# Performance work log

Hardware: AMD Instinct MI355X
Metric: run time of the kernel (lower is better)

The kernel has to match this reference:

```python
import jax, jax.numpy as jnp
import numpy as np

B, T, F = 256, 784, 1
H, D, C = 256, 1024, 10  # cell_size, dense_size, num_classes


def setup_inputs() -> dict:
    key = jax.random.key(0)
    ks = jax.random.split(key, 5)
    s = 0.05
    return {
        "X": jax.random.normal(ks[0], (B, T, F), jnp.float32),
        "W_lstm": jax.random.normal(ks[1], (F + H, 4 * H), jnp.float32) * s,
        "b_lstm": jnp.zeros((4 * H,), jnp.float32),
        "W_dense": jax.random.normal(ks[2], (H, D), jnp.float32) * s,
        "b_dense": jnp.zeros((D,), jnp.float32),
        "W_pred": jax.random.normal(ks[3], (D, C), jnp.float32) * s,
        "b_pred": jnp.zeros((C,), jnp.float32),
        "seq_length": T,
    }


def reference(X, W_lstm, b_lstm, W_dense, b_dense, W_pred, b_pred, seq_length):
    # TF LSTMCell: kernel [F+H, 4H], gate order (i, j, f, o), forget_bias=1.0
    b, t, f = X.shape
    h4 = W_lstm.shape[1]
    h = h4 // 4
    Wx, Wh = W_lstm[:f], W_lstm[f:]
    # Precompute input projections for all timesteps: [T, B, 4H]
    xproj = jnp.einsum('tbf,fg->tbg', jnp.transpose(X, (1, 0, 2)), Wx) + b_lstm

    def step(carry, xp):
        c, hst = carry
        gates = xp + hst @ Wh  # [B, 4H]
        i, j, fg, o = jnp.split(gates, 4, axis=-1)
        new_c = jax.nn.sigmoid(fg + 1.0) * c + jax.nn.sigmoid(i) * jnp.tanh(j)
        new_h = jax.nn.sigmoid(o) * jnp.tanh(new_c)
        return (new_c, new_h), None

    init = (jnp.zeros((b, h), X.dtype), jnp.zeros((b, h), X.dtype))
    (_, h_last), _ = jax.lax.scan(step, init, xproj)

    # Dropout in inference mode = identity
    dense = jax.nn.relu(h_last @ W_dense + b_dense)
    logits = dense @ W_pred + b_pred
    return logits
```

## Files before the change

### kernel.cpp

```cpp
#include <hip/hip_runtime.h>
#include <stdint.h>

#define TSEQ  784
#define BATCH 256
#define HID   256
#define DNS   1024
#define NCLS  10
#define NGRP  16
#define NSLC  8

typedef __attribute__((ext_vector_type(8))) short bf16x8_t;
typedef __attribute__((ext_vector_type(4))) float f32x4_t;

__device__ __forceinline__ float sigmoidf_(float x) { return 1.0f / (1.0f + __expf(-x)); }
__device__ __forceinline__ float tanhf_(float x) {
    float ax = fabsf(x);
    float e  = __expf(2.0f * ax);
    float r  = 1.0f - 2.0f / (e + 1.0f);
    return copysignf(r, x);
}
__device__ __forceinline__ uint32_t bf16rne(float f) {
    uint32_t u = __float_as_uint(f);
    return (u + 0x7FFFu + ((u >> 16) & 1u)) >> 16;
}
__device__ __forceinline__ float bf16tof(uint32_t h) { return __uint_as_float(h << 16); }

__global__ __launch_bounds__(256, 1)
void lstm_mfma(const float* __restrict__ X,
               const float* __restrict__ W_lstm,
               const float* __restrict__ b_lstm,
               uint32_t* __restrict__ hx,
               uint32_t* __restrict__ tags)
{
    __shared__ uint32_t WtU[32768];
    __shared__ uint32_t hA[4096];
    __shared__ float    gateL[4 * 32 * 17];

    const int tid  = threadIdx.x;
    const int lane = tid & 63;
    const int wid  = tid >> 6;
    const int cidx = lane & 15;
    const int kh   = lane >> 4;

    const int bid = blockIdx.x;
    const int s   = bid >> 4;
    const int g   = bid & 15;

    for (int idx = tid; idx < 8 * 16 * 128; idx += 256) {
        const int n  = idx >> 11;
        const int c  = (idx >> 7) & 15;
        const int dw = idx & 127;
        const int k0 = dw * 2;
        const int col = (n >> 1) * 256 + s * 32 + (n & 1) * 16 + c;
        const float w0 = W_lstm[(1 + k0) * 1024 + col];
        const float w1 = W_lstm[(2 + k0) * 1024 + col];
        const uint32_t h0 = bf16rne(w0), h1 = bf16rne(w1);
        const uint32_t l0 = bf16rne(w0 - bf16tof(h0));
        const uint32_t l1 = bf16rne(w1 - bf16tof(h1));
        const int kc = dw >> 2, rem = dw & 3;
        const int dwp = ((kc ^ (c & 7)) << 2) | rem;
        const int o = (n * 16 + c) * 128 + dwp;
        WtU[o]         = h0 | (h1 << 16);
        WtU[16384 + o] = l0 | (l1 << 16);
    }

    const int er = tid >> 4;
    const int eu = tid & 15;
    float wx0[4], wx1[4], bb0[4], bb1[4];
    #pragma unroll
    for (int q = 0; q < 4; ++q) {
        const int c0 = q * 256 + s * 32 + eu;
        wx0[q] = W_lstm[c0];      wx1[q] = W_lstm[c0 + 16];
        bb0[q] = b_lstm[c0];      bb1[q] = b_lstm[c0 + 16];
    }
    const float* xrow = X + (g * 16 + er) * TSEQ;
    float cc0 = 0.0f, cc1 = 0.0f;

    const int key = (cidx + (cidx >> 2)) & 3;
    const int kq  = (kh ^ key) << 2;

    __syncthreads();

    bf16x8_t Bh0[8], Bl0[8], Bh1[8], Bl1[8];
    #pragma unroll
    for (int kt = 0; kt < 8; ++kt) {
        const int kc  = kt * 4 + kh;
        const int ob0 = ((wid * 2) * 16 + cidx) * 128 + ((kc ^ (cidx & 7)) << 2);
        const int ob1 = ((wid * 2 + 1) * 16 + cidx) * 128 + ((kc ^ (cidx & 7)) << 2);
        Bh0[kt] = *reinterpret_cast<const bf16x8_t*>(&WtU[ob0]);
        Bl0[kt] = *reinterpret_cast<const bf16x8_t*>(&WtU[16384 + ob0]);
        Bh1[kt] = *reinterpret_cast<const bf16x8_t*>(&WtU[ob1]);
        Bl1[kt] = *reinterpret_cast<const bf16x8_t*>(&WtU[16384 + ob1]);
    }

    for (int t = 0; t < TSEQ; ++t) {
        #pragma unroll
        for (int kt = 0; kt < 8; kt += 4) {
            asm volatile("" : "+v"(Bh0[kt]), "+v"(Bh0[kt+1]), "+v"(Bh0[kt+2]), "+v"(Bh0[kt+3]),
                              "+v"(Bl0[kt]), "+v"(Bl0[kt+1]), "+v"(Bl0[kt+2]), "+v"(Bl0[kt+3]));
            asm volatile("" : "+v"(Bh1[kt]), "+v"(Bh1[kt+1]), "+v"(Bh1[kt+2]), "+v"(Bh1[kt+3]),
                              "+v"(Bl1[kt]), "+v"(Bl1[kt+1]), "+v"(Bl1[kt+2]), "+v"(Bl1[kt+3]));
        }

        if (t > 0 && wid == 0) {
            const uint32_t tt = (uint32_t)t;
            int guard = 1 << 22;
            bool ok;
            do {
                uint32_t v = __hip_atomic_load(&tags[g * 8 + (lane & 7)],
                                               __ATOMIC_RELAXED, __HIP_MEMORY_SCOPE_AGENT);
                ok = __all(v >= tt);
            } while (!ok && --guard);
        }
        __syncthreads();

        {
            const int bufr = t & 1;
            const unsigned long long* src =
                (const unsigned long long*)hx + (size_t)(bufr * NGRP + g) * 2048;
            unsigned long long v[8];
            #pragma unroll
            for (int j = 0; j < 8; ++j) {
                v[j] = __hip_atomic_load(&src[j * 256 + tid],
                                         __ATOMIC_RELAXED, __HIP_MEMORY_SCOPE_AGENT);
            }
            #pragma unroll
            for (int j = 0; j < 8; ++j) {
                const int m   = j * 256 + tid;
                const int kt  = m >> 8;
                const int lvl = (m >> 7) & 1;
                const int ci  = (m & 127) >> 3;
                const int ko  = (m & 7) * 2;
                const int khj = ko >> 2, dp = ko & 3;
                const int kyj = (ci + (ci >> 2)) & 3;
                const int dst = kt * 512 + lvl * 256 + ci * 16 + ((khj ^ kyj) << 2) + dp;
                *(unsigned long long*)&hA[dst] = v[j];
            }
        }
        __syncthreads();

        f32x4_t acc0 = {0.f, 0.f, 0.f, 0.f}, acc1 = acc0;
        #pragma unroll
        for (int kt = 0; kt < 8; ++kt) {
            bf16x8_t av_h = *reinterpret_cast<const bf16x8_t*>(&hA[kt * 512 + cidx * 16 + kq]);
            bf16x8_t av_l = *reinterpret_cast<const bf16x8_t*>(&hA[kt * 512 + 256 + cidx * 16 + kq]);
            acc0 = __builtin_amdgcn_mfma_f32_16x16x32_bf16(av_h, Bh0[kt], acc0, 0, 0, 0);
            acc0 = __builtin_amdgcn_mfma_f32_16x16x32_bf16(av_h, Bl0[kt], acc0, 0, 0, 0);
            acc0 = __builtin_amdgcn_mfma_f32_16x16x32_bf16(av_l, Bh0[kt], acc0, 0, 0, 0);
            acc1 = __builtin_amdgcn_mfma_f32_16x16x32_bf16(av_h, Bh1[kt], acc1, 0, 0, 0);
            acc1 = __builtin_amdgcn_mfma_f32_16x16x32_bf16(av_h, Bl1[kt], acc1, 0, 0, 0);
            acc1 = __builtin_amdgcn_mfma_f32_16x16x32_bf16(av_l, Bh1[kt], acc1, 0, 0, 0);
        }

        #pragma unroll
        for (int reg = 0; reg < 4; ++reg) {
            gateL[(wid * 32 + cidx) * 17      + kh * 4 + reg] = acc0[reg];
            gateL[(wid * 32 + 16 + cidx) * 17 + kh * 4 + reg] = acc1[reg];
        }
        __syncthreads();

        const float xv = xrow[t];
        float g0[4], g1[4];
        #pragma unroll
        for (int q = 0; q < 4; ++q) {
            g0[q] = gateL[(q * 32 + eu) * 17 + er]      + xv * wx0[q] + bb0[q];
            g1[q] = gateL[(q * 32 + 16 + eu) * 17 + er] + xv * wx1[q] + bb1[q];
        }
        cc0 = fmaf(sigmoidf_(g0[2] + 1.0f), cc0, sigmoidf_(g0[0]) * tanhf_(g0[1]));
        const float h0 = sigmoidf_(g0[3]) * tanhf_(cc0);
        cc1 = fmaf(sigmoidf_(g1[2] + 1.0f), cc1, sigmoidf_(g1[0]) * tanhf_(g1[1]));
        const float h1 = sigmoidf_(g1[3]) * tanhf_(cc1);

        const float h0n = __shfl_xor(h0, 1, 64);
        const float h1n = __shfl_xor(h1, 1, 64);
        if ((eu & 1) == 0) {
            const int bufw  = (t + 1) & 1;
            const int basew = ((bufw * NGRP + g) * NSLC + s) * 512 + er * 16;
            const uint32_t hi0 = bf16rne(h0),  hi0n = bf16rne(h0n);
            const uint32_t hi1 = bf16rne(h1),  hi1n = bf16rne(h1n);
            const uint32_t lo0  = bf16rne(h0  - bf16tof(hi0));
            const uint32_t lo0n = bf16rne(h0n - bf16tof(hi0n));
            const uint32_t lo1  = bf16rne(h1  - bf16tof(hi1));
            const uint32_t lo1n = bf16rne(h1n - bf16tof(hi1n));
            const int D0 = eu >> 1, D1 = 8 + (eu >> 1);
            __hip_atomic_store(&hx[basew + D0], hi0 | (hi0n << 16),
                               __ATOMIC_RELAXED, __HIP_MEMORY_SCOPE_AGENT);
            __hip_atomic_store(&hx[basew + D1], hi1 | (hi1n << 16),
                               __ATOMIC_RELAXED, __HIP_MEMORY_SCOPE_AGENT);
            __hip_atomic_store(&hx[basew + 256 + D0], lo0 | (lo0n << 16),
                               __ATOMIC_RELAXED, __HIP_MEMORY_SCOPE_AGENT);
            __hip_atomic_store(&hx[basew + 256 + D1], lo1 | (lo1n << 16),
                               __ATOMIC_RELAXED, __HIP_MEMORY_SCOPE_AGENT);
        }
        __syncthreads();
        if (tid == 0) {
            __hip_atomic_store(&tags[g * 8 + s], (uint32_t)(t + 1),
                               __ATOMIC_RELAXED, __HIP_MEMORY_SCOPE_AGENT);
        }
    }
}

__global__ __launch_bounds__(256, 1)
void head_kernel(const uint32_t* __restrict__ hx,
                 const float* __restrict__ W_dense,
                 const float* __restrict__ b_dense,
                 const float* __restrict__ W_pred,
                 const float* __restrict__ b_pred,
                 float* __restrict__ out) {
    __shared__ float hs[HID];
    __shared__ float ds[DNS];
    __shared__ float red[4];

    const int b = blockIdx.x;
    const int g = b >> 4, er = b & 15;
    const int tid = threadIdx.x;

    {
        const int s  = tid >> 5;
        const int uu = tid & 31;
        const int base = (g * NSLC + s) * 512 + er * 16;
        const uint32_t dh = __hip_atomic_load(&hx[base + (uu >> 1)],
                                              __ATOMIC_RELAXED, __HIP_MEMORY_SCOPE_AGENT);
        const uint32_t dl = __hip_atomic_load(&hx[base + 256 + (uu >> 1)],
                                              __ATOMIC_RELAXED, __HIP_MEMORY_SCOPE_AGENT);
        const int sh = (uu & 1) * 16;
        hs[tid] = bf16tof((dh >> sh) & 0xFFFFu) + bf16tof((dl >> sh) & 0xFFFFu);
    }
    __syncthreads();

    for (int d = tid; d < DNS; d += 256) {
        float acc = b_dense[d];
        for (int k = 0; k < HID; k += 4) {
            float4 h4 = *reinterpret_cast<const float4*>(&hs[k]);
            acc = fmaf(h4.x, W_dense[(k + 0) * DNS + d], acc);
            acc = fmaf(h4.y, W_dense[(k + 1) * DNS + d], acc);
            acc = fmaf(h4.z, W_dense[(k + 2) * DNS + d], acc);
            acc = fmaf(h4.w, W_dense[(k + 3) * DNS + d], acc);
        }
        ds[d] = fmaxf(acc, 0.0f);
    }
    __syncthreads();

    const int wid = tid >> 6, lane = tid & 63;
    for (int c = 0; c < NCLS; ++c) {
        float p = 0.0f;
        for (int k = tid; k < DNS; k += 256) {
            p = fmaf(ds[k], W_pred[k * NCLS + c], p);
        }
        #pragma unroll
        for (int off = 32; off > 0; off >>= 1) {
            p += __shfl_down(p, off, 64);
        }
        if (lane == 0) red[wid] = p;
        __syncthreads();
        if (tid == 0) {
            out[b * NCLS + c] = red[0] + red[1] + red[2] + red[3] + b_pred[c];
        }
        __syncthreads();
    }
}

extern "C" void kernel_launch(void* const* d_in, const int* in_sizes, int n_in,
                              void* d_out, int out_size, void* d_ws, size_t ws_size,
                              hipStream_t stream) {
    const float* X       = (const float*)d_in[0];
    const float* W_lstm  = (const float*)d_in[1];
    const float* b_lstm  = (const float*)d_in[2];
    const float* W_dense = (const float*)d_in[3];
    const float* b_dense = (const float*)d_in[4];
    const float* W_pred  = (const float*)d_in[5];
    const float* b_pred  = (const float*)d_in[6];
    float* out = (float*)d_out;

    uint32_t* hx   = (uint32_t*)d_ws;
    uint32_t* tags = hx + 131072;

    hipMemsetAsync(hx, 0, NGRP * NSLC * 512 * sizeof(uint32_t), stream);
    hipMemsetAsync(tags, 0, NGRP * NSLC * sizeof(uint32_t), stream);

    lstm_mfma<<<NGRP * NSLC, 256, 0, stream>>>(X, W_lstm, b_lstm, hx, tags);
    head_kernel<<<BATCH, 256, 0, stream>>>(hx, W_dense, b_dense, W_pred, b_pred, out);
}
```

Baseline: 2.127 ms.

## Transpose gate accumulators in registers via lane shuffles instead of LDS round-trip

Reorders the recurrent weight columns so that each MFMA output tile holds all four gates for a small set of units. A 4x4 register transpose built from cross-lane shuffles then gives each lane its i/j/f/o values directly. This removes the shared-memory gate staging buffer and one block-wide barrier per timestep on the serial recurrence. In exchange it adds shuffle and select instructions and changes which lane owns which batch row and unit.

```diff
diff --git a/kernel.cpp b/kernel.cpp
--- a/kernel.cpp
+++ b/kernel.cpp
@@ -24,6 +24,30 @@
     return (u + 0x7FFFu + ((u >> 16) & 1u)) >> 16;
 }
 __device__ __forceinline__ float bf16tof(uint32_t h) { return __uint_as_float(h << 16); }
+
+__device__ __forceinline__ f32x4_t xpose44(f32x4_t M, int p) {
+    const bool pb1 = (p & 2) != 0;
+    float s0 = pb1 ? M[0] : M[2];
+    float s1 = pb1 ? M[1] : M[3];
+    float r0 = __shfl_xor(s0, 8, 64);
+    float r1 = __shfl_xor(s1, 8, 64);
+    f32x4_t N;
+    N[0] = pb1 ? r0 : M[0];
+    N[1] = pb1 ? r1 : M[1];
+    N[2] = pb1 ? M[2] : r0;
+    N[3] = pb1 ? M[3] : r1;
+    const bool pb0 = (p & 1) != 0;
+    s0 = pb0 ? N[0] : N[1];
+    s1 = pb0 ? N[2] : N[3];
+    r0 = __shfl_xor(s0, 4, 64);
+    r1 = __shfl_xor(s1, 4, 64);
+    f32x4_t T;
+    T[0] = pb0 ? r0 : N[0];
+    T[1] = pb0 ? N[1] : r0;
+    T[2] = pb0 ? r1 : N[2];
+    T[3] = pb0 ? N[3] : r1;
+    return T;
+}
 
 __global__ __launch_bounds__(256, 1)
 void lstm_mfma(const float* __restrict__ X,
@@ -34,7 +58,6 @@
 {
     __shared__ uint32_t WtU[32768];
     __shared__ uint32_t hA[4096];
-    __shared__ float    gateL[4 * 32 * 17];
 
     const int tid  = threadIdx.x;
     const int lane = tid & 63;
@@ -51,7 +74,7 @@
         const int c  = (idx >> 7) & 15;
         const int dw = idx & 127;
         const int k0 = dw * 2;
-        const int col = (n >> 1) * 256 + s * 32 + (n & 1) * 16 + c;
+        const int col = (c >> 2) * 256 + s * 32 + n * 4 + (c & 3);
         const float w0 = W_lstm[(1 + k0) * 1024 + col];
         const float w1 = W_lstm[(2 + k0) * 1024 + col];
         const uint32_t h0 = bf16rne(w0), h1 = bf16rne(w1);
@@ -64,17 +87,20 @@
         WtU[16384 + o] = l0 | (l1 << 16);
     }
 
-    const int er = tid >> 4;
-    const int eu = tid & 15;
-    float wx0[4], wx1[4], bb0[4], bb1[4];
+    const int p     = cidx >> 2;
+    const int row   = kh * 4 + p;
+    const int unitA = 8 * wid + (cidx & 3);
+    const int unitB = unitA + 4;
+    float wxA[4], wxB[4], bbA[4], bbB[4];
     #pragma unroll
     for (int q = 0; q < 4; ++q) {
-        const int c0 = q * 256 + s * 32 + eu;
-        wx0[q] = W_lstm[c0];      wx1[q] = W_lstm[c0 + 16];
-        bb0[q] = b_lstm[c0];      bb1[q] = b_lstm[c0 + 16];
-    }
-    const float* xrow = X + (g * 16 + er) * TSEQ;
-    float cc0 = 0.0f, cc1 = 0.0f;
+        wxA[q] = W_lstm[q * 256 + s * 32 + unitA];
+        wxB[q] = W_lstm[q * 256 + s * 32 + unitB];
+        bbA[q] = b_lstm[q * 256 + s * 32 + unitA];
+        bbB[q] = b_lstm[q * 256 + s * 32 + unitB];
+    }
+    const float* xrowp = X + (g * 16 + row) * TSEQ;
+    float ccA = 0.0f, ccB = 0.0f;
 
     const int key = (cidx + (cidx >> 2)) & 3;
     const int kq  = (kh ^ key) << 2;
@@ -152,44 +178,41 @@
             acc1 = __builtin_amdgcn_mfma_f32_16x16x32_bf16(av_l, Bh1[kt], acc1, 0, 0, 0);
         }
 
-        #pragma unroll
-        for (int reg = 0; reg < 4; ++reg) {
-            gateL[(wid * 32 + cidx) * 17      + kh * 4 + reg] = acc0[reg];
-            gateL[(wid * 32 + 16 + cidx) * 17 + kh * 4 + reg] = acc1[reg];
-        }
-        __syncthreads();
-
-        const float xv = xrow[t];
-        float g0[4], g1[4];
+        f32x4_t TA = xpose44(acc0, p);
+        f32x4_t TB = xpose44(acc1, p);
+
+        const float xv = xrowp[t];
+        float gA[4], gB[4];
         #pragma unroll
         for (int q = 0; q < 4; ++q) {
-            g0[q] = gateL[(q * 32 + eu) * 17 + er]      + xv * wx0[q] + bb0[q];
-            g1[q] = gateL[(q * 32 + 16 + eu) * 17 + er] + xv * wx1[q] + bb1[q];
-        }
-        cc0 = fmaf(sigmoidf_(g0[2] + 1.0f), cc0, sigmoidf_(g0[0]) * tanhf_(g0[1]));
-        const float h0 = sigmoidf_(g0[3]) * tanhf_(cc0);
-        cc1 = fmaf(sigmoidf_(g1[2] + 1.0f), cc1, sigmoidf_(g1[0]) * tanhf_(g1[1]));
-        const float h1 = sigmoidf_(g1[3]) * tanhf_(cc1);
+            gA[q] = TA[q] + xv * wxA[q] + bbA[q];
+            gB[q] = TB[q] + xv * wxB[q] + bbB[q];
+        }
+        ccA = fmaf(sigmoidf_(gA[2] + 1.0f), ccA, sigmoidf_(gA[0]) * tanhf_(gA[1]));
+        const float h0 = sigmoidf_(gA[3]) * tanhf_(ccA);
+        ccB = fmaf(sigmoidf_(gB[2] + 1.0f), ccB, sigmoidf_(gB[0]) * tanhf_(gB[1]));
+        const float h1 = sigmoidf_(gB[3]) * tanhf_(ccB);
 
         const float h0n = __shfl_xor(h0, 1, 64);
         const float h1n = __shfl_xor(h1, 1, 64);
-        if ((eu & 1) == 0) {
+        if ((cidx & 1) == 0) {
             const int bufw  = (t + 1) & 1;
-            const int basew = ((bufw * NGRP + g) * NSLC + s) * 512 + er * 16;
+            const int basew = ((bufw * NGRP + g) * NSLC + s) * 512 + row * 16;
             const uint32_t hi0 = bf16rne(h0),  hi0n = bf16rne(h0n);
             const uint32_t hi1 = bf16rne(h1),  hi1n = bf16rne(h1n);
             const uint32_t lo0  = bf16rne(h0  - bf16tof(hi0));
             const uint32_t lo0n = bf16rne(h0n - bf16tof(hi0n));
             const uint32_t lo1  = bf16rne(h1  - bf16tof(hi1));
             const uint32_t lo1n = bf16rne(h1n - bf16tof(hi1n));
-            const int D0 = eu >> 1, D1 = 8 + (eu >> 1);
-            __hip_atomic_store(&hx[basew + D0], hi0 | (hi0n << 16),
-                               __ATOMIC_RELAXED, __HIP_MEMORY_SCOPE_AGENT);
-            __hip_atomic_store(&hx[basew + D1], hi1 | (hi1n << 16),
-                               __ATOMIC_RELAXED, __HIP_MEMORY_SCOPE_AGENT);
-            __hip_atomic_store(&hx[basew + 256 + D0], lo0 | (lo0n << 16),
-                               __ATOMIC_RELAXED, __HIP_MEMORY_SCOPE_AGENT);
-            __hip_atomic_store(&hx[basew + 256 + D1], lo1 | (lo1n << 16),
+            const int DA = unitA >> 1;
+            const int DB = unitB >> 1;
+            __hip_atomic_store(&hx[basew + DA], hi0 | (hi0n << 16),
+                               __ATOMIC_RELAXED, __HIP_MEMORY_SCOPE_AGENT);
+            __hip_atomic_store(&hx[basew + DB], hi1 | (hi1n << 16),
+                               __ATOMIC_RELAXED, __HIP_MEMORY_SCOPE_AGENT);
+            __hip_atomic_store(&hx[basew + 256 + DA], lo0 | (lo0n << 16),
+                               __ATOMIC_RELAXED, __HIP_MEMORY_SCOPE_AGENT);
+            __hip_atomic_store(&hx[basew + 256 + DB], lo1 | (lo1n << 16),
                                __ATOMIC_RELAXED, __HIP_MEMORY_SCOPE_AGENT);
         }
         __syncthreads();
```

Result: slower. 2.267 ms (+6.6%).
